# Optimization experiments

Measured on AMD Instinct MI355X. Metric: run time of the kernel, lower is better.

Reference implementation:

```python
import jax, jax.numpy as jnp
import numpy as np
from jax import lax

B, T, INPUT, HIDDEN, OUT = 8192, 512, 10, 64, 1


def setup_inputs() -> dict:
    key = jax.random.key(0)
    k1, k2, k3, k4, k5 = jax.random.split(key, 5)
    padded_batch = jax.random.normal(k1, (B, T, INPUT), dtype=jnp.float32)
    lengths = jax.random.randint(k2, (B,), 1, T + 1, dtype=jnp.int64)
    # per-timestep distinct RNN weights, init scale 0.01 as in the torch module
    W_xh = jax.random.normal(k3, (T, INPUT, HIDDEN), dtype=jnp.float32) * 0.01
    W_hh = jax.random.normal(k4, (T, HIDDEN, HIDDEN), dtype=jnp.float32) * 0.01
    W_lin = jax.random.normal(k5, (HIDDEN, OUT), dtype=jnp.float32) * (1.0 / np.sqrt(HIDDEN))
    b_lin = jnp.zeros((OUT,), dtype=jnp.float32)
    return {"padded_batch": padded_batch, "lengths": lengths,
            "W_xh": W_xh, "W_hh": W_hh, "W_lin": W_lin, "b_lin": b_lin}


def reference(padded_batch, lengths, W_xh, W_hh, W_lin, b_lin):
    # padded_batch: [B, T, INPUT]; per-step weights W_xh: [T, INPUT, H], W_hh: [T, H, H]
    Bn = padded_batch.shape[0]
    x_tbd = jnp.swapaxes(padded_batch, 0, 1)  # [T, B, INPUT]
    t_idx = jnp.arange(T)

    def step(h, inputs):
        x_t, wxh, whh, t = inputs
        new_h = jnp.tanh(x_t @ wxh + h @ whh)          # [B, H]
        keep = (t < lengths)[:, None]                   # freeze samples past their length
        h = jnp.where(keep, new_h, h)
        return h, None

    h0 = jnp.zeros((Bn, HIDDEN), dtype=padded_batch.dtype)
    last_hidden, _ = lax.scan(step, h0, (x_tbd, W_xh, W_hh, t_idx))
    return last_hidden @ W_lin + b_lin  # [B, OUT]
```

## Files before the change

kernel.cpp:

```cpp
#include <hip/hip_runtime.h>
#include <stdint.h>

#define T_STEPS 512
#define HID     64
#define INP     10
#define MB      16
#define KS      88
#define HS      72
#define XS      40
#define WT_ELEMS (HID*KS)
#define WT_BYTES (WT_ELEMS*2)
#define WS_SLOTS (WT_BYTES/16)
#define WB_SLOTS 768
#define WB_ELEMS (WB_SLOTS*8)

typedef float  f32x4  __attribute__((ext_vector_type(4)));
typedef short  s16x8  __attribute__((ext_vector_type(8)));
typedef __bf16 bf16x8 __attribute__((ext_vector_type(8)));

typedef const __attribute__((address_space(1))) unsigned int* gp_t;
typedef __attribute__((address_space(3))) unsigned int*       lp_t;

__device__ __forceinline__ short f2bf(float f) {
    unsigned u = __builtin_bit_cast(unsigned, f);
    u = (u + 0x7FFFu + ((u >> 16) & 1u)) >> 16;
    return (short)u;
}
__device__ __forceinline__ short f2bfh(float f) {
    return __builtin_bit_cast(short, (__bf16)f);
}
__device__ __forceinline__ float bf2f(short s) {
    unsigned u = ((unsigned)(unsigned short)s) << 16;
    return __builtin_bit_cast(float, u);
}

__global__ __launch_bounds__(256) void prep_w(const float* __restrict__ Wxh,
                                              const float* __restrict__ Whh,
                                              short* __restrict__ Wc) {
    __shared__ float s_hh[64 * 65];
    __shared__ float s_xh[INP * 65];
    const int t = blockIdx.x, tid = threadIdx.x;
    for (int i = tid; i < 64 * 64; i += 256)
        s_hh[(i >> 6) * 65 + (i & 63)] = Whh[t * 4096 + i];
    for (int i = tid; i < INP * 64; i += 256)
        s_xh[(i >> 6) * 65 + (i & 63)] = Wxh[t * (INP * 64) + i];
    __syncthreads();
    short* dst = Wc + (size_t)t * WT_ELEMS;
    for (int i = tid; i < WT_ELEMS; i += 256) {
        const int n = i / KS, k = i % KS;
        float v = 0.f;
        if (k < 64)      v = s_hh[k * 65 + n];
        else if (k < 74) v = s_xh[(k - 64) * 65 + n];
        dst[i] = f2bf(v);
    }
}

__global__ __launch_bounds__(256, 2) void rnn_main(const float* __restrict__ X,
                                                   const int* __restrict__ L,
                                                   const short* __restrict__ Wc,
                                                   const float* __restrict__ Wlin,
                                                   const float* __restrict__ blin,
                                                   float* __restrict__ out) {
    __shared__ __attribute__((aligned(16))) short Wb[3][WB_ELEMS];
    __shared__ __attribute__((aligned(16))) short hb[2][MB * HS];
    __shared__ __attribute__((aligned(16))) short xb[2][MB * XS];
    __shared__ __attribute__((aligned(16))) float xf[4][256];
    __shared__ int len_s[MB];

    const int tid  = threadIdx.x;
    const int lane = tid & 63;
    const int wv   = tid >> 6;
    const int q    = lane >> 4;
    const int l    = lane & 15;
    const long long bbase = (long long)blockIdx.x * MB;

    const int ws2_src = (((tid + 512) < WS_SLOTS) ? (tid + 512) : 0) * 16;
    auto issue_w = [&](int tp, int buf) {
        const char* src = (const char*)Wc + (size_t)tp * WT_BYTES;
        char* dst = (char*)&Wb[buf][0];
        __builtin_amdgcn_global_load_lds((gp_t)(src + tid * 16),
                                         (lp_t)(dst + tid * 16), 16, 0, 0);
        __builtin_amdgcn_global_load_lds((gp_t)(src + (tid + 256) * 16),
                                         (lp_t)(dst + (tid + 256) * 16), 16, 0, 0);
        __builtin_amdgcn_global_load_lds((gp_t)(src + ws2_src),
                                         (lp_t)(dst + (tid + 512) * 16), 16, 0, 0);
    };

    const int s47   = (lane < 48) ? lane : 47;
    const int xrow  = s47 / 3;
    const int xpart = s47 - xrow * 3;
    const int xpoff = (xpart == 0) ? 0 : ((xpart == 1) ? 8 : 24);
    const char* xsrc0 = (const char*)X + (size_t)(bbase + xrow) * (T_STEPS * INP * 4) + xpoff;
    auto issue_xf = [&](int tx, int buf) {
        __builtin_amdgcn_global_load_lds((gp_t)(xsrc0 + (size_t)tx * (INP * 4)),
                                         (lp_t)((char*)&xf[buf][0] + lane * 16), 16, 0, 0);
    };

    const int xs = tid / INP, xi = tid % INP;
    const int xfoff = xs * 48 + xi * 4 + (xi < 4 ? 0 : 8);

    if (tid < MB) len_s[tid] = L[bbase + tid];
    for (int i = tid; i < MB * HS; i += 256) hb[0][i] = 0;
    for (int i = tid; i < MB * XS; i += 256) { xb[0][i] = 0; xb[1][i] = 0; }

    issue_w(0, 0);
    issue_xf(0, 0);
    issue_xf(1, 1);
    issue_w(1, 1);
    issue_xf(2, 2);
    asm volatile("s_waitcnt vmcnt(4)" ::: "memory");
    __builtin_amdgcn_sched_barrier(0);
    if (tid < MB * INP) {
        const float x0 = *(const float*)((const char*)&xf[0][0] + xfoff);
        xb[0][xs * XS + xi] = f2bfh(x0);
    }
    asm volatile("s_waitcnt lgkmcnt(0)" ::: "memory");
    __builtin_amdgcn_s_barrier();

    float hc[4] = {0.f, 0.f, 0.f, 0.f};
    int len4[4];
#pragma unroll
    for (int r = 0; r < 4; ++r) len4[r] = len_s[q * 4 + r];
    const int colw = wv * 16 + l;
    const int woff = colw * KS + q * 8;

    int rb = 0;

    for (int t = 0; t < T_STEPS; ++t) {
        const int cur = t & 1, nxt = cur ^ 1;
        const int pb  = (rb >= 1) ? rb - 1 : 2;

        const int tpw = (t + 2 < T_STEPS) ? t + 2 : T_STEPS - 1;
        const int tpx = (t + 3 < T_STEPS) ? t + 3 : T_STEPS - 1;
        issue_w(tpw, pb);
        issue_xf(tpx, (t + 3) & 3);

        if (tid < MB * INP) {
            const float xv = *(const float*)((const char*)&xf[(t + 1) & 3][0] + xfoff);
            xb[nxt][xs * XS + xi] = f2bfh(xv);
        }
        const s16x8 a0 = *(const s16x8*)&hb[cur][l * HS + q * 8];
        const s16x8 a1 = *(const s16x8*)&hb[cur][l * HS + 32 + q * 8];
        const s16x8 a2 = *(const s16x8*)&xb[cur][l * XS + q * 8];
        const s16x8 b0 = *(const s16x8*)&Wb[rb][woff];
        const s16x8 b1 = *(const s16x8*)&Wb[rb][woff + 32];
        const s16x8 b2 = *(const s16x8*)&Wb[rb][woff + 64];

        f32x4 z = {0.f, 0.f, 0.f, 0.f};
        f32x4 acc0 = __builtin_amdgcn_mfma_f32_16x16x32_bf16(
                  __builtin_bit_cast(bf16x8, a0), __builtin_bit_cast(bf16x8, b0), z, 0, 0, 0);
        f32x4 acc1 = __builtin_amdgcn_mfma_f32_16x16x32_bf16(
                  __builtin_bit_cast(bf16x8, a1), __builtin_bit_cast(bf16x8, b1), z, 0, 0, 0);
        f32x4 acc2 = __builtin_amdgcn_mfma_f32_16x16x32_bf16(
                  __builtin_bit_cast(bf16x8, a2), __builtin_bit_cast(bf16x8, b2), z, 0, 0, 0);

#pragma unroll
        for (int r = 0; r < 4; ++r) {
            const float a  = acc0[r] + acc1[r] + acc2[r];
            const float e  = __expf(2.f * a);
            const float th = 1.f - 2.f * __builtin_amdgcn_rcpf(e + 1.f);
            hc[r] = (t < len4[r]) ? th : hc[r];
            hb[nxt][(q * 4 + r) * HS + colw] = f2bfh(hc[r]);
        }

        asm volatile("s_waitcnt vmcnt(4)");
        asm volatile("s_waitcnt lgkmcnt(0)" ::: "memory");
        __builtin_amdgcn_s_barrier();

        rb = (rb == 2) ? 0 : rb + 1;
    }

    asm volatile("s_waitcnt vmcnt(0)" ::: "memory");

    const float wl = Wlin[lane];
    const float bl = blin[0];
#pragma unroll
    for (int it = 0; it < 4; ++it) {
        const int s = wv + it * 4;
        float v = bf2f(hb[0][s * HS + lane]) * wl;
#pragma unroll
        for (int off = 32; off > 0; off >>= 1) v += __shfl_down(v, off);
        if (lane == 0) out[bbase + s] = v + bl;
    }
}

extern "C" void kernel_launch(void* const* d_in, const int* in_sizes, int n_in,
                              void* d_out, int out_size, void* d_ws, size_t ws_size,
                              hipStream_t stream) {
    const float* X    = (const float*)d_in[0];
    const int*   L    = (const int*)d_in[1];
    const float* Wxh  = (const float*)d_in[2];
    const float* Whh  = (const float*)d_in[3];
    const float* Wlin = (const float*)d_in[4];
    const float* blin = (const float*)d_in[5];
    float*       out  = (float*)d_out;
    short*       Wc   = (short*)d_ws;

    prep_w<<<T_STEPS, 256, 0, stream>>>(Wxh, Whh, Wc);
    rnn_main<<<8192 / MB, 256, 0, stream>>>(X, L, Wc, Wlin, blin, out);
}
```

Before: 637.1 us.

## Process 32 samples per block with 8 waves, double-buffer weights, load x via registers

Doubles the batch tile per block to 32 samples with 512 threads, so each per-step weight matrix loaded into LDS serves twice as many rows and total weight traffic is halved. The triple-buffered weight prefetch two steps ahead becomes a double buffer fetched one step ahead, and the x prefetch moves from LDS staging into plain global loads held in registers. Synchronisation is now a full __syncthreads per step, and the shorter prefetch distance may expose global-load latency on the serial recurrence chain. The grid is halved to 256 blocks, which leaves fewer blocks per CU.

```diff
diff --git a/kernel.cpp b/kernel.cpp
--- a/kernel.cpp
+++ b/kernel.cpp
@@ -4,15 +4,14 @@
 #define T_STEPS 512
 #define HID     64
 #define INP     10
-#define MB      16
+#define MB      32
+#define NTHR    512
 #define KS      88
 #define HS      72
 #define XS      40
 #define WT_ELEMS (HID*KS)
 #define WT_BYTES (WT_ELEMS*2)
 #define WS_SLOTS (WT_BYTES/16)
-#define WB_SLOTS 768
-#define WB_ELEMS (WB_SLOTS*8)
 
 typedef float  f32x4  __attribute__((ext_vector_type(4)));
 typedef short  s16x8  __attribute__((ext_vector_type(8)));
@@ -55,96 +54,74 @@
     }
 }
 
-__global__ __launch_bounds__(256, 2) void rnn_main(const float* __restrict__ X,
-                                                   const int* __restrict__ L,
-                                                   const short* __restrict__ Wc,
-                                                   const float* __restrict__ Wlin,
-                                                   const float* __restrict__ blin,
-                                                   float* __restrict__ out) {
-    __shared__ __attribute__((aligned(16))) short Wb[3][WB_ELEMS];
+__global__ __launch_bounds__(NTHR, 2) void rnn_main(const float* __restrict__ X,
+                                                    const int* __restrict__ L,
+                                                    const short* __restrict__ Wc,
+                                                    const float* __restrict__ Wlin,
+                                                    const float* __restrict__ blin,
+                                                    float* __restrict__ out) {
+    __shared__ __attribute__((aligned(16))) short Wb[2][WT_ELEMS + 16];
     __shared__ __attribute__((aligned(16))) short hb[2][MB * HS];
     __shared__ __attribute__((aligned(16))) short xb[2][MB * XS];
-    __shared__ __attribute__((aligned(16))) float xf[4][256];
     __shared__ int len_s[MB];
 
     const int tid  = threadIdx.x;
     const int lane = tid & 63;
-    const int wv   = tid >> 6;
+    const int w    = tid >> 6;
+    const int mt   = w >> 2;
+    const int nt   = w & 3;
     const int q    = lane >> 4;
     const int l    = lane & 15;
     const long long bbase = (long long)blockIdx.x * MB;
 
-    const int ws2_src = (((tid + 512) < WS_SLOTS) ? (tid + 512) : 0) * 16;
-    auto issue_w = [&](int tp, int buf) {
+    auto issue_w = [&](int tp) {
         const char* src = (const char*)Wc + (size_t)tp * WT_BYTES;
-        char* dst = (char*)&Wb[buf][0];
+        char* dst = (char*)&Wb[tp & 1][0];
         __builtin_amdgcn_global_load_lds((gp_t)(src + tid * 16),
                                          (lp_t)(dst + tid * 16), 16, 0, 0);
-        __builtin_amdgcn_global_load_lds((gp_t)(src + (tid + 256) * 16),
-                                         (lp_t)(dst + (tid + 256) * 16), 16, 0, 0);
-        __builtin_amdgcn_global_load_lds((gp_t)(src + ws2_src),
-                                         (lp_t)(dst + (tid + 512) * 16), 16, 0, 0);
+        if (tid < WS_SLOTS - 512)
+            __builtin_amdgcn_global_load_lds((gp_t)(src + (tid + 512) * 16),
+                                             (lp_t)(dst + (tid + 512) * 16), 16, 0, 0);
     };
 
-    const int s47   = (lane < 48) ? lane : 47;
-    const int xrow  = s47 / 3;
-    const int xpart = s47 - xrow * 3;
-    const int xpoff = (xpart == 0) ? 0 : ((xpart == 1) ? 8 : 24);
-    const char* xsrc0 = (const char*)X + (size_t)(bbase + xrow) * (T_STEPS * INP * 4) + xpoff;
-    auto issue_xf = [&](int tx, int buf) {
-        __builtin_amdgcn_global_load_lds((gp_t)(xsrc0 + (size_t)tx * (INP * 4)),
-                                         (lp_t)((char*)&xf[buf][0] + lane * 16), 16, 0, 0);
-    };
-
-    const int xs = tid / INP, xi = tid % INP;
-    const int xfoff = xs * 48 + xi * 4 + (xi < 4 ? 0 : 8);
+    const int xs = tid / INP, xi = tid - (tid / INP) * INP;
 
     if (tid < MB) len_s[tid] = L[bbase + tid];
-    for (int i = tid; i < MB * HS; i += 256) hb[0][i] = 0;
-    for (int i = tid; i < MB * XS; i += 256) { xb[0][i] = 0; xb[1][i] = 0; }
+    for (int i = tid; i < MB * HS; i += NTHR) hb[0][i] = 0;
+    for (int i = tid; i < MB * XS; i += NTHR) { xb[0][i] = 0; xb[1][i] = 0; }
+    if (tid < 16) { Wb[0][WT_ELEMS + tid] = 0; Wb[1][WT_ELEMS + tid] = 0; }
+    issue_w(0);
+    __syncthreads();
 
-    issue_w(0, 0);
-    issue_xf(0, 0);
-    issue_xf(1, 1);
-    issue_w(1, 1);
-    issue_xf(2, 2);
-    asm volatile("s_waitcnt vmcnt(4)" ::: "memory");
-    __builtin_amdgcn_sched_barrier(0);
+    float xrA = 0.f, xrB = 0.f;
     if (tid < MB * INP) {
-        const float x0 = *(const float*)((const char*)&xf[0][0] + xfoff);
-        xb[0][xs * XS + xi] = f2bfh(x0);
+        xb[0][xs * XS + xi] = f2bfh(X[(bbase + xs) * (T_STEPS * INP) + 0 * INP + xi]);
+        xrA = X[(bbase + xs) * (T_STEPS * INP) + 1 * INP + xi];
     }
-    asm volatile("s_waitcnt lgkmcnt(0)" ::: "memory");
-    __builtin_amdgcn_s_barrier();
+    __syncthreads();
 
     float hc[4] = {0.f, 0.f, 0.f, 0.f};
     int len4[4];
 #pragma unroll
-    for (int r = 0; r < 4; ++r) len4[r] = len_s[q * 4 + r];
-    const int colw = wv * 16 + l;
+    for (int r = 0; r < 4; ++r) len4[r] = len_s[mt * 16 + q * 4 + r];
+    const int colw = nt * 16 + l;
     const int woff = colw * KS + q * 8;
+    const int arow = mt * 16 + l;
 
-    int rb = 0;
+    auto stepf = [&](int t, float& xr_held, float& xr_new) {
+        const int cur = t & 1, nxt = cur ^ 1;
 
-    for (int t = 0; t < T_STEPS; ++t) {
-        const int cur = t & 1, nxt = cur ^ 1;
-        const int pb  = (rb >= 1) ? rb - 1 : 2;
+        if (tid < MB * INP && t + 2 < T_STEPS)
+            xr_new = X[(bbase + xs) * (T_STEPS * INP) + (long long)(t + 2) * INP + xi];
+        if (t + 1 < T_STEPS) issue_w(t + 1);
+        if (tid < MB * INP) xb[nxt][xs * XS + xi] = f2bfh(xr_held);
 
-        const int tpw = (t + 2 < T_STEPS) ? t + 2 : T_STEPS - 1;
-        const int tpx = (t + 3 < T_STEPS) ? t + 3 : T_STEPS - 1;
-        issue_w(tpw, pb);
-        issue_xf(tpx, (t + 3) & 3);
-
-        if (tid < MB * INP) {
-            const float xv = *(const float*)((const char*)&xf[(t + 1) & 3][0] + xfoff);
-            xb[nxt][xs * XS + xi] = f2bfh(xv);
-        }
-        const s16x8 a0 = *(const s16x8*)&hb[cur][l * HS + q * 8];
-        const s16x8 a1 = *(const s16x8*)&hb[cur][l * HS + 32 + q * 8];
-        const s16x8 a2 = *(const s16x8*)&xb[cur][l * XS + q * 8];
-        const s16x8 b0 = *(const s16x8*)&Wb[rb][woff];
-        const s16x8 b1 = *(const s16x8*)&Wb[rb][woff + 32];
-        const s16x8 b2 = *(const s16x8*)&Wb[rb][woff + 64];
+        const s16x8 a0 = *(const s16x8*)&hb[cur][arow * HS + q * 8];
+        const s16x8 a1 = *(const s16x8*)&hb[cur][arow * HS + 32 + q * 8];
+        const s16x8 a2 = *(const s16x8*)&xb[cur][arow * XS + q * 8];
+        const s16x8 b0 = *(const s16x8*)&Wb[cur][woff];
+        const s16x8 b1 = *(const s16x8*)&Wb[cur][woff + 32];
+        const s16x8 b2 = *(const s16x8*)&Wb[cur][woff + 64];
 
         f32x4 z = {0.f, 0.f, 0.f, 0.f};
         f32x4 acc0 = __builtin_amdgcn_mfma_f32_16x16x32_bf16(
@@ -160,23 +137,21 @@
             const float e  = __expf(2.f * a);
             const float th = 1.f - 2.f * __builtin_amdgcn_rcpf(e + 1.f);
             hc[r] = (t < len4[r]) ? th : hc[r];
-            hb[nxt][(q * 4 + r) * HS + colw] = f2bfh(hc[r]);
+            hb[nxt][(mt * 16 + q * 4 + r) * HS + colw] = f2bfh(hc[r]);
         }
+        __syncthreads();
+    };
 
-        asm volatile("s_waitcnt vmcnt(4)");
-        asm volatile("s_waitcnt lgkmcnt(0)" ::: "memory");
-        __builtin_amdgcn_s_barrier();
-
-        rb = (rb == 2) ? 0 : rb + 1;
+    for (int tt = 0; tt < T_STEPS; tt += 2) {
+        stepf(tt,     xrA, xrB);
+        stepf(tt + 1, xrB, xrA);
     }
-
-    asm volatile("s_waitcnt vmcnt(0)" ::: "memory");
 
     const float wl = Wlin[lane];
     const float bl = blin[0];
 #pragma unroll
     for (int it = 0; it < 4; ++it) {
-        const int s = wv + it * 4;
+        const int s = w + it * 8;
         float v = bf2f(hb[0][s * HS + lane]) * wl;
 #pragma unroll
         for (int off = 32; off > 0; off >>= 1) v += __shfl_down(v, off);
@@ -197,5 +172,5 @@
     short*       Wc   = (short*)d_ws;
 
     prep_w<<<T_STEPS, 256, 0, stream>>>(Wxh, Whh, Wc);
-    rnn_main<<<8192 / MB, 256, 0, stream>>>(X, L, Wc, Wlin, blin, out);
+    rnn_main<<<8192 / MB, NTHR, 0, stream>>>(X, L, Wc, Wlin, blin, out);
 }
```

Result: faster. 537.2 us (-15.7%).
